# Performance work log

Hardware: AMD Instinct MI355X
Metric: run time of the kernel (lower is better)

Reference implementation:

```python
import jax, jax.numpy as jnp
import numpy as np

IN_FEATURES = 4096
OUT_FEATURES = 4096
BATCH, SEQ = 8, 2048


def setup_inputs() -> dict:
    key = jax.random.key(0)
    k1, k2, k3, k4 = jax.random.split(key, 4)
    x = jax.random.normal(k1, (BATCH, SEQ, IN_FEATURES), dtype=jnp.float32)
    # packed int4 weights: each int8 byte holds two signed 4-bit values
    weight = jax.random.randint(k2, (OUT_FEATURES, IN_FEATURES // 2), -128, 128, dtype=jnp.int8)
    # per-output-row symmetric quant scales (positive, small)
    scales = jax.random.uniform(k3, (OUT_FEATURES,), dtype=jnp.float32, minval=0.005, maxval=0.02)
    bias = jax.random.normal(k4, (OUT_FEATURES,), dtype=jnp.float32)
    return {"x": x, "weight": weight, "scales": scales, "bias": bias}


def _dequant_int4(weight, scales):
    # low nibble -> even input columns, high nibble -> odd input columns.
    # Arithmetic shifts on int8 sign-extend the 4-bit values.
    low = jnp.right_shift(jnp.left_shift(weight, 4), 4)   # (O, I/2) in [-8, 7]
    high = jnp.right_shift(weight, 4)                      # (O, I/2) in [-8, 7]
    w = jnp.stack([low, high], axis=-1).reshape(weight.shape[0], -1)  # (O, I)
    return w.astype(jnp.float32) * scales[:, None]


def reference(x, weight, scales, bias):
    W = _dequant_int4(weight, scales)                      # (O, I) fp32
    # y[b,s,o] = sum_i x[b,s,i] * W[o,i] + bias[o]
    return jnp.einsum('bsi,oi->bso', x, W) + bias
```

## Files before the change

kernel.cpp:

```cpp
#include <hip/hip_runtime.h>
#include <hip/hip_bf16.h>
#include <stdint.h>

#define M_TOTAL 16384
#define N_TOTAL 4096
#define K_TOTAL 4096

#define BM 256
#define BN 256
#define BKI 128
#define NTI (K_TOTAL / BKI)

typedef __attribute__((ext_vector_type(4))) float f32x4;
typedef __attribute__((ext_vector_type(4))) int   i32x4;
typedef __attribute__((ext_vector_type(2))) int   i32x2;

__global__ __launch_bounds__(256) void quant_x_kernel(
    const float* __restrict__ x, signed char* __restrict__ xq,
    float* __restrict__ qrow) {
  __shared__ float red[8];
  const int row = blockIdx.x;
  const int tid = threadIdx.x;
  const float* xr = x + (size_t)row * K_TOTAL;
  const f32x4* xv = (const f32x4*)xr;

  f32x4 v[4];
  float mx = 0.f;
#pragma unroll
  for (int j = 0; j < 4; ++j) {
    v[j] = xv[j * 256 + tid];
#pragma unroll
    for (int e = 0; e < 4; ++e) mx = fmaxf(mx, fabsf(v[j][e]));
  }
#pragma unroll
  for (int off = 32; off > 0; off >>= 1) mx = fmaxf(mx, __shfl_xor(mx, off));
  if ((tid & 63) == 0) red[tid >> 6] = mx;
  __syncthreads();
  if (tid == 0) {
    float m2 = fmaxf(fmaxf(red[0], red[1]), fmaxf(red[2], red[3]));
    red[4] = m2;
    qrow[row] = m2 * (1.f / 127.f);
  }
  __syncthreads();
  const float rmax = red[4];
  const float rq = rmax > 0.f ? 127.f / rmax : 0.f;

  int* oq = (int*)(xq + (size_t)row * K_TOTAL);
#pragma unroll
  for (int j = 0; j < 4; ++j) {
    int b0 = (int)rintf(v[j][0] * rq) & 0xff;
    int b1 = (int)rintf(v[j][1] * rq) & 0xff;
    int b2 = (int)rintf(v[j][2] * rq) & 0xff;
    int b3 = (int)rintf(v[j][3] * rq) & 0xff;
    oq[j * 256 + tid] = b0 | (b1 << 8) | (b2 << 16) | (b3 << 24);
  }
}

__global__ void dequant_w8_kernel(const int* __restrict__ wq,
                                  signed char* __restrict__ w8) {
  const int n = (N_TOTAL * (K_TOTAL / 2)) / 4;
  int idx = blockIdx.x * blockDim.x + threadIdx.x;
  int stride = gridDim.x * blockDim.x;
  const i32x4* wv = (const i32x4*)wq;
  i32x2* ov = (i32x2*)w8;
  for (int i = idx; i < n; i += stride) {
    i32x4 w = wv[i];
    int words[2];
#pragma unroll
    for (int h = 0; h < 2; ++h) {
      int b0 = w[2 * h], b1 = w[2 * h + 1];
      int lo0 = (((b0 & 0xF) ^ 8) - 8) & 0xff;
      int hi0 = ((((b0 >> 4) & 0xF) ^ 8) - 8) & 0xff;
      int lo1 = (((b1 & 0xF) ^ 8) - 8) & 0xff;
      int hi1 = ((((b1 >> 4) & 0xF) ^ 8) - 8) & 0xff;
      words[h] = lo0 | (hi0 << 8) | (lo1 << 16) | (hi1 << 24);
    }
    i32x2 o; o[0] = words[0]; o[1] = words[1];
    ov[i] = o;
  }
}

#define MFMAI(a, b, c) __builtin_amdgcn_mfma_i32_16x16x64_i8((a), (b), (c), 0, 0, 0)
#define SCHED0() __builtin_amdgcn_sched_barrier(0)

__global__ __launch_bounds__(512, 2) void gemm256_i8_kernel(
    const signed char* __restrict__ A8,
    const signed char* __restrict__ B8,
    const float* __restrict__ qrow,
    const float* __restrict__ scales,
    const float* __restrict__ bias,
    float* __restrict__ C) {
  __shared__ signed char lds[2][2][BM * BKI];

  const int t  = threadIdx.x;
  const int l  = t & 63;
  const int w  = t >> 6;
  const int wm = w >> 2;
  const int wn = w & 3;
  const int fr = l & 15;
  const int kg = l >> 4;
  const int sx = fr & 7;

  const int wg = blockIdx.x;
  const int bm = (wg & 7) * 8 + ((wg >> 3) & 7);
  const int bn = wg >> 6;

  const int rr   = t >> 3;
  const int ssrc = (t & 7) ^ (rr & 7);
  const signed char* pa = A8 + (size_t)(bm * BM + rr) * K_TOTAL + ssrc * 16;
  const signed char* pb = B8 + (size_t)(bn * BN + rr) * K_TOTAL + ssrc * 16;

#define GLL(gp, lp) __builtin_amdgcn_global_load_lds( \
      (const __attribute__((address_space(1))) unsigned int*)(gp), \
      (__attribute__((address_space(3))) unsigned int*)(lp), 16, 0, 0)

  auto stage = [&](int buf, int kt) {
#pragma unroll
    for (int g = 0; g < 4; ++g)
      GLL(pa + (size_t)g * 64 * K_TOTAL + kt, &lds[buf][0][g * 8192 + t * 16]);
#pragma unroll
    for (int g = 0; g < 4; ++g)
      GLL(pb + (size_t)g * 64 * K_TOTAL + kt, &lds[buf][1][g * 8192 + t * 16]);
  };

  i32x4 acc[8][4] = {};

  stage(0, 0);
  stage(1, BKI);

  const int so0 = (kg ^ sx) * 16;
  const int so1 = ((4 + kg) ^ sx) * 16;

  for (int t0 = 0; t0 < NTI; ++t0) {
    if (t0 == NTI - 1) { asm volatile("s_waitcnt vmcnt(0)" ::: "memory"); }
    else               { asm volatile("s_waitcnt vmcnt(8)" ::: "memory"); }
    SCHED0();
    __builtin_amdgcn_s_barrier();
    SCHED0();

    const int cur = t0 & 1;
    const signed char* Abp = &lds[cur][0][(wm * 128 + fr) * BKI];
    const signed char* Bbp = &lds[cur][1][(wn * 64 + fr) * BKI];

    i32x4 b[4][2], alo[4][2], ahi[4][2];
#pragma unroll
    for (int kk = 0; kk < 2; ++kk) {
      const int so = kk ? so1 : so0;
#pragma unroll
      for (int n = 0; n < 4; ++n) b[n][kk]   = *(const i32x4*)&Bbp[n * 16 * BKI + so];
#pragma unroll
      for (int m = 0; m < 4; ++m) alo[m][kk] = *(const i32x4*)&Abp[m * 16 * BKI + so];
    }
    SCHED0();
#pragma unroll
    for (int kk = 0; kk < 2; ++kk) {
      const int so = kk ? so1 : so0;
#pragma unroll
      for (int m = 0; m < 4; ++m) ahi[m][kk] = *(const i32x4*)&Abp[(m + 4) * 16 * BKI + so];
    }
    SCHED0();
    asm volatile("s_waitcnt lgkmcnt(8)" ::: "memory");
    SCHED0();
    __builtin_amdgcn_s_setprio(1);
#pragma unroll
    for (int kk = 0; kk < 2; ++kk)
#pragma unroll
      for (int m = 0; m < 4; ++m)
#pragma unroll
        for (int n = 0; n < 4; ++n)
          acc[m][n] = MFMAI(alo[m][kk], b[n][kk], acc[m][n]);
    __builtin_amdgcn_s_setprio(0);
    SCHED0();
    asm volatile("s_waitcnt lgkmcnt(0)" ::: "memory");
    SCHED0();
    __builtin_amdgcn_s_barrier();
    SCHED0();

    if (t0 + 2 < NTI) stage(cur, (t0 + 2) * BKI);

    __builtin_amdgcn_s_setprio(1);
#pragma unroll
    for (int kk = 0; kk < 2; ++kk)
#pragma unroll
      for (int m = 0; m < 4; ++m)
#pragma unroll
        for (int n = 0; n < 4; ++n)
          acc[m + 4][n] = MFMAI(ahi[m][kk], b[n][kk], acc[m + 4][n]);
    __builtin_amdgcn_s_setprio(0);
    SCHED0();
  }

  const int row0 = bm * BM + wm * 128 + kg * 4;
  const int col0 = bn * BN + wn * 64 + fr;
  float qv[8][4];
#pragma unroll
  for (int m = 0; m < 8; ++m)
#pragma unroll
    for (int r = 0; r < 4; ++r) qv[m][r] = qrow[row0 + m * 16 + r];
#pragma unroll
  for (int n = 0; n < 4; ++n) {
    const int gc = col0 + n * 16;
    const float s  = scales[gc];
    const float bv = bias[gc];
#pragma unroll
    for (int m = 0; m < 8; ++m) {
      const int gr = row0 + m * 16;
#pragma unroll
      for (int r = 0; r < 4; ++r)
        C[(size_t)(gr + r) * N_TOTAL + gc] = (float)acc[m][n][r] * (qv[m][r] * s) + bv;
    }
  }
#undef GLL
}

__global__ void naive_int4_kernel(const float* __restrict__ x,
                                  const int* __restrict__ wq,
                                  const float* __restrict__ scales,
                                  const float* __restrict__ bias,
                                  float* __restrict__ out) {
  size_t idx = (size_t)blockIdx.x * blockDim.x + threadIdx.x;
  int o = (int)(idx & (N_TOTAL - 1));
  int m = (int)(idx >> 12);
  const float* xr = x + (size_t)m * K_TOTAL;
  const int* wrow = wq + (size_t)o * (K_TOTAL / 2);
  float acc = 0.f;
  for (int j = 0; j < K_TOTAL / 2; ++j) {
    int b = wrow[j];
    int lo = ((b & 0xF) ^ 8) - 8;
    int hi = (((b >> 4) & 0xF) ^ 8) - 8;
    acc += xr[2 * j] * (float)lo + xr[2 * j + 1] * (float)hi;
  }
  out[idx] = acc * scales[o] + bias[o];
}

extern "C" void kernel_launch(void* const* d_in, const int* in_sizes, int n_in,
                              void* d_out, int out_size, void* d_ws, size_t ws_size,
                              hipStream_t stream) {
  const float* x      = (const float*)d_in[0];
  const int*   wq     = (const int*)d_in[1];
  const float* scales = (const float*)d_in[2];
  const float* bias   = (const float*)d_in[3];
  float* out = (float*)d_out;

  const size_t needXQ = (size_t)M_TOTAL * K_TOTAL;
  const size_t needW8 = (size_t)N_TOTAL * K_TOTAL;
  const size_t needQ  = (size_t)M_TOTAL * sizeof(float);

  if (d_ws != nullptr && ws_size >= needXQ + needW8 + needQ) {
    signed char* xq = (signed char*)d_ws;
    signed char* w8 = (signed char*)d_ws + needXQ;
    float* qrow = (float*)((char*)d_ws + needXQ + needW8);
    quant_x_kernel<<<M_TOTAL, 256, 0, stream>>>(x, xq, qrow);
    dequant_w8_kernel<<<1024, 256, 0, stream>>>(wq, w8);
    gemm256_i8_kernel<<<(M_TOTAL / BM) * (N_TOTAL / BN), 512, 0, stream>>>(
        xq, w8, qrow, scales, bias, out);
  } else {
    const size_t total = (size_t)M_TOTAL * N_TOTAL;
    naive_int4_kernel<<<(unsigned)(total / 256), 256, 0, stream>>>(x, wq, scales, bias, out);
  }
}
```

Baseline: 341.9 us.

## Load A operand directly from global into registers, stage only B in LDS

```diff
diff --git a/kernel.cpp b/kernel.cpp
--- a/kernel.cpp
+++ b/kernel.cpp
@@ -90,7 +90,7 @@
     const float* __restrict__ scales,
     const float* __restrict__ bias,
     float* __restrict__ C) {
-  __shared__ signed char lds[2][2][BM * BKI];
+  __shared__ signed char ldsB[2][BN * BKI];
 
   const int t  = threadIdx.x;
   const int l  = t & 63;
@@ -107,86 +107,101 @@
 
   const int rr   = t >> 3;
   const int ssrc = (t & 7) ^ (rr & 7);
-  const signed char* pa = A8 + (size_t)(bm * BM + rr) * K_TOTAL + ssrc * 16;
   const signed char* pb = B8 + (size_t)(bn * BN + rr) * K_TOTAL + ssrc * 16;
 
 #define GLL(gp, lp) __builtin_amdgcn_global_load_lds( \
       (const __attribute__((address_space(1))) unsigned int*)(gp), \
       (__attribute__((address_space(3))) unsigned int*)(lp), 16, 0, 0)
 
-  auto stage = [&](int buf, int kt) {
+  auto stageB = [&](int buf, int kt) {
 #pragma unroll
     for (int g = 0; g < 4; ++g)
-      GLL(pa + (size_t)g * 64 * K_TOTAL + kt, &lds[buf][0][g * 8192 + t * 16]);
-#pragma unroll
-    for (int g = 0; g < 4; ++g)
-      GLL(pb + (size_t)g * 64 * K_TOTAL + kt, &lds[buf][1][g * 8192 + t * 16]);
+      GLL(pb + (size_t)g * 64 * K_TOTAL + kt, &ldsB[buf][g * 8192 + t * 16]);
   };
 
+  const signed char* pA = A8 + (size_t)(bm * BM + wm * 128 + fr) * K_TOTAL + kg * 16;
+
   i32x4 acc[8][4] = {};
-
-  stage(0, 0);
-  stage(1, BKI);
+  i32x4 a0[8], a1[8], b[4][2];
+
+  stageB(0, 0);
+  stageB(1, BKI);
+#pragma unroll
+  for (int mf = 0; mf < 8; ++mf)
+    a0[mf] = *(const i32x4*)(pA + (size_t)mf * 16 * K_TOTAL);
+#pragma unroll
+  for (int mf = 0; mf < 8; ++mf)
+    a1[mf] = *(const i32x4*)(pA + (size_t)mf * 16 * K_TOTAL + 64);
+  SCHED0();
 
   const int so0 = (kg ^ sx) * 16;
   const int so1 = ((4 + kg) ^ sx) * 16;
 
   for (int t0 = 0; t0 < NTI; ++t0) {
-    if (t0 == NTI - 1) { asm volatile("s_waitcnt vmcnt(0)" ::: "memory"); }
-    else               { asm volatile("s_waitcnt vmcnt(8)" ::: "memory"); }
+    const bool hasNext = (t0 + 1 < NTI);
+    const size_t ktn = (size_t)(t0 + 1) * BKI;
+
+    asm volatile("s_waitcnt vmcnt(16)" ::: "memory");
     SCHED0();
     __builtin_amdgcn_s_barrier();
     SCHED0();
 
     const int cur = t0 & 1;
-    const signed char* Abp = &lds[cur][0][(wm * 128 + fr) * BKI];
-    const signed char* Bbp = &lds[cur][1][(wn * 64 + fr) * BKI];
-
-    i32x4 b[4][2], alo[4][2], ahi[4][2];
-#pragma unroll
-    for (int kk = 0; kk < 2; ++kk) {
-      const int so = kk ? so1 : so0;
-#pragma unroll
-      for (int n = 0; n < 4; ++n) b[n][kk]   = *(const i32x4*)&Bbp[n * 16 * BKI + so];
-#pragma unroll
-      for (int m = 0; m < 4; ++m) alo[m][kk] = *(const i32x4*)&Abp[m * 16 * BKI + so];
-    }
-    SCHED0();
-#pragma unroll
-    for (int kk = 0; kk < 2; ++kk) {
-      const int so = kk ? so1 : so0;
-#pragma unroll
-      for (int m = 0; m < 4; ++m) ahi[m][kk] = *(const i32x4*)&Abp[(m + 4) * 16 * BKI + so];
-    }
-    SCHED0();
-    asm volatile("s_waitcnt lgkmcnt(8)" ::: "memory");
-    SCHED0();
+    const signed char* Bbp = &ldsB[cur][(wn * 64 + fr) * BKI];
+
+#pragma unroll
+    for (int n = 0; n < 4; ++n) b[n][0] = *(const i32x4*)&Bbp[n * 16 * BKI + so0];
+    SCHED0();
+#pragma unroll
+    for (int n = 0; n < 4; ++n) b[n][1] = *(const i32x4*)&Bbp[n * 16 * BKI + so1];
+    SCHED0();
+
     __builtin_amdgcn_s_setprio(1);
 #pragma unroll
-    for (int kk = 0; kk < 2; ++kk)
-#pragma unroll
-      for (int m = 0; m < 4; ++m)
-#pragma unroll
-        for (int n = 0; n < 4; ++n)
-          acc[m][n] = MFMAI(alo[m][kk], b[n][kk], acc[m][n]);
+    for (int m = 0; m < 8; ++m)
+#pragma unroll
+      for (int n = 0; n < 4; ++n)
+        acc[m][n] = MFMAI(a0[m], b[n][0], acc[m][n]);
     __builtin_amdgcn_s_setprio(0);
     SCHED0();
+
+    if (hasNext) {
+#pragma unroll
+      for (int mf = 0; mf < 8; ++mf)
+        a0[mf] = *(const i32x4*)(pA + (size_t)mf * 16 * K_TOTAL + ktn);
+    }
+    SCHED0();
+
+    __builtin_amdgcn_s_setprio(1);
+#pragma unroll
+    for (int m = 0; m < 8; ++m)
+#pragma unroll
+      for (int n = 0; n < 4; ++n)
+        acc[m][n + 0] = acc[m][n];
+    __builtin_amdgcn_s_setprio(0);
+#pragma unroll
+    for (int m = 0; m < 8; ++m) { }
+    __builtin_amdgcn_s_setprio(1);
+#pragma unroll
+    for (int m = 0; m < 8; ++m)
+#pragma unroll
+      for (int n = 0; n < 4; ++n)
+        acc[m][n] = MFMAI(a1[m], b[n][1], acc[m][n]);
+    __builtin_amdgcn_s_setprio(0);
+    SCHED0();
+
     asm volatile("s_waitcnt lgkmcnt(0)" ::: "memory");
     SCHED0();
     __builtin_amdgcn_s_barrier();
     SCHED0();
 
-    if (t0 + 2 < NTI) stage(cur, (t0 + 2) * BKI);
-
-    __builtin_amdgcn_s_setprio(1);
-#pragma unroll
-    for (int kk = 0; kk < 2; ++kk)
-#pragma unroll
-      for (int m = 0; m < 4; ++m)
-#pragma unroll
-        for (int n = 0; n < 4; ++n)
-          acc[m + 4][n] = MFMAI(ahi[m][kk], b[n][kk], acc[m + 4][n]);
-    __builtin_amdgcn_s_setprio(0);
+    if (t0 + 2 < NTI) stageB(cur, (size_t)(t0 + 2) * BKI);
+    SCHED0();
+    if (hasNext) {
+#pragma unroll
+      for (int mf = 0; mf < 8; ++mf)
+        a1[mf] = *(const i32x4*)(pA + (size_t)mf * 16 * K_TOTAL + ktn + 64);
+    }
     SCHED0();
   }
 
```

After: 636.7 us. 86.2% more time.

## Switch int8 GEMM to 4-stage pipeline with 64-wide K tiles and one barrier

Applied to the files above, without the earlier changes.

```diff
diff --git a/kernel.cpp b/kernel.cpp
--- a/kernel.cpp
+++ b/kernel.cpp
@@ -8,7 +8,7 @@
 
 #define BM 256
 #define BN 256
-#define BKI 128
+#define BKI 64
 #define NTI (K_TOTAL / BKI)
 
 typedef __attribute__((ext_vector_type(4))) float f32x4;
@@ -90,7 +90,7 @@
     const float* __restrict__ scales,
     const float* __restrict__ bias,
     float* __restrict__ C) {
-  __shared__ signed char lds[2][2][BM * BKI];
+  __shared__ signed char lds[4][2][BM * BKI];
 
   const int t  = threadIdx.x;
   const int l  = t & 63;
@@ -99,96 +99,71 @@
   const int wn = w & 3;
   const int fr = l & 15;
   const int kg = l >> 4;
-  const int sx = fr & 7;
+  const int sxs = (kg ^ ((fr >> 1) & 3)) << 4;
 
   const int wg = blockIdx.x;
   const int bm = (wg & 7) * 8 + ((wg >> 3) & 7);
   const int bn = wg >> 6;
 
-  const int rr   = t >> 3;
-  const int ssrc = (t & 7) ^ (rr & 7);
-  const signed char* pa = A8 + (size_t)(bm * BM + rr) * K_TOTAL + ssrc * 16;
-  const signed char* pb = B8 + (size_t)(bn * BN + rr) * K_TOTAL + ssrc * 16;
+  const int rr   = t >> 2;
+  const int ssrc = ((t & 3) ^ ((t >> 3) & 3)) << 4;
+  const signed char* pa = A8 + (size_t)(bm * BM + rr) * K_TOTAL + ssrc;
+  const signed char* pb = B8 + (size_t)(bn * BN + rr) * K_TOTAL + ssrc;
 
 #define GLL(gp, lp) __builtin_amdgcn_global_load_lds( \
       (const __attribute__((address_space(1))) unsigned int*)(gp), \
       (__attribute__((address_space(3))) unsigned int*)(lp), 16, 0, 0)
 
-  auto stage = [&](int buf, int kt) {
-#pragma unroll
-    for (int g = 0; g < 4; ++g)
-      GLL(pa + (size_t)g * 64 * K_TOTAL + kt, &lds[buf][0][g * 8192 + t * 16]);
-#pragma unroll
-    for (int g = 0; g < 4; ++g)
-      GLL(pb + (size_t)g * 64 * K_TOTAL + kt, &lds[buf][1][g * 8192 + t * 16]);
+  auto stage = [&](int slot, size_t kt) {
+    GLL(pa + kt,                           &lds[slot][0][t * 16]);
+    GLL(pa + (size_t)128 * K_TOTAL + kt,   &lds[slot][0][8192 + t * 16]);
+    GLL(pb + kt,                           &lds[slot][1][t * 16]);
+    GLL(pb + (size_t)128 * K_TOTAL + kt,   &lds[slot][1][8192 + t * 16]);
   };
 
   i32x4 acc[8][4] = {};
 
-  stage(0, 0);
-  stage(1, BKI);
-
-  const int so0 = (kg ^ sx) * 16;
-  const int so1 = ((4 + kg) ^ sx) * 16;
-
-  for (int t0 = 0; t0 < NTI; ++t0) {
-    if (t0 == NTI - 1) { asm volatile("s_waitcnt vmcnt(0)" ::: "memory"); }
-    else               { asm volatile("s_waitcnt vmcnt(8)" ::: "memory"); }
-    SCHED0();
-    __builtin_amdgcn_s_barrier();
-    SCHED0();
-
-    const int cur = t0 & 1;
-    const signed char* Abp = &lds[cur][0][(wm * 128 + fr) * BKI];
-    const signed char* Bbp = &lds[cur][1][(wn * 64 + fr) * BKI];
-
-    i32x4 b[4][2], alo[4][2], ahi[4][2];
-#pragma unroll
-    for (int kk = 0; kk < 2; ++kk) {
-      const int so = kk ? so1 : so0;
-#pragma unroll
-      for (int n = 0; n < 4; ++n) b[n][kk]   = *(const i32x4*)&Bbp[n * 16 * BKI + so];
-#pragma unroll
-      for (int m = 0; m < 4; ++m) alo[m][kk] = *(const i32x4*)&Abp[m * 16 * BKI + so];
-    }
-    SCHED0();
-#pragma unroll
-    for (int kk = 0; kk < 2; ++kk) {
-      const int so = kk ? so1 : so0;
-#pragma unroll
-      for (int m = 0; m < 4; ++m) ahi[m][kk] = *(const i32x4*)&Abp[(m + 4) * 16 * BKI + so];
-    }
-    SCHED0();
-    asm volatile("s_waitcnt lgkmcnt(8)" ::: "memory");
-    SCHED0();
-    __builtin_amdgcn_s_setprio(1);
-#pragma unroll
-    for (int kk = 0; kk < 2; ++kk)
-#pragma unroll
-      for (int m = 0; m < 4; ++m)
-#pragma unroll
-        for (int n = 0; n < 4; ++n)
-          acc[m][n] = MFMAI(alo[m][kk], b[n][kk], acc[m][n]);
-    __builtin_amdgcn_s_setprio(0);
-    SCHED0();
-    asm volatile("s_waitcnt lgkmcnt(0)" ::: "memory");
-    SCHED0();
-    __builtin_amdgcn_s_barrier();
-    SCHED0();
-
-    if (t0 + 2 < NTI) stage(cur, (t0 + 2) * BKI);
-
-    __builtin_amdgcn_s_setprio(1);
-#pragma unroll
-    for (int kk = 0; kk < 2; ++kk)
-#pragma unroll
-      for (int m = 0; m < 4; ++m)
-#pragma unroll
-        for (int n = 0; n < 4; ++n)
-          acc[m + 4][n] = MFMAI(ahi[m][kk], b[n][kk], acc[m + 4][n]);
-    __builtin_amdgcn_s_setprio(0);
-    SCHED0();
-  }
+  const int abase = (wm * 128 + fr) * BKI + sxs;
+  const int bbase = (wn * 64 + fr) * BKI + sxs;
+
+  stage(0, 0); stage(1, BKI); stage(2, 2 * BKI);
+  asm volatile("s_waitcnt vmcnt(8)" ::: "memory");
+  SCHED0();
+  __builtin_amdgcn_s_barrier();
+  SCHED0();
+
+#define TILE_BODY(T0, DOSTAGE, VMASM) do {                                   \
+    const signed char* Ab = &lds[(T0) & 3][0][abase];                        \
+    const signed char* Bb = &lds[(T0) & 3][1][bbase];                        \
+    i32x4 a_[8], b_[4];                                                      \
+    _Pragma("unroll")                                                        \
+    for (int mf = 0; mf < 8; ++mf) a_[mf] = *(const i32x4*)&Ab[mf * 16 * BKI]; \
+    _Pragma("unroll")                                                        \
+    for (int nf = 0; nf < 4; ++nf) b_[nf] = *(const i32x4*)&Bb[nf * 16 * BKI]; \
+    SCHED0();                                                                \
+    if (DOSTAGE) stage(((T0) + 3) & 3, (size_t)((T0) + 3) * BKI);            \
+    SCHED0();                                                                \
+    asm volatile(VMASM ::: "memory");                                        \
+    asm volatile("s_waitcnt lgkmcnt(0)" ::: "memory");                       \
+    SCHED0();                                                                \
+    __builtin_amdgcn_s_barrier();                                            \
+    SCHED0();                                                                \
+    __builtin_amdgcn_s_setprio(1);                                           \
+    _Pragma("unroll")                                                        \
+    for (int mf = 0; mf < 8; ++mf)                                           \
+      _Pragma("unroll")                                                      \
+      for (int nf = 0; nf < 4; ++nf)                                         \
+        acc[mf][nf] = MFMAI(a_[mf], b_[nf], acc[mf][nf]);                    \
+    __builtin_amdgcn_s_setprio(0);                                           \
+    SCHED0();                                                                \
+  } while (0)
+
+  for (int t0 = 0; t0 < NTI - 3; ++t0)
+    TILE_BODY(t0, true, "s_waitcnt vmcnt(8)");
+  TILE_BODY(NTI - 3, false, "s_waitcnt vmcnt(4)");
+  TILE_BODY(NTI - 2, false, "s_waitcnt vmcnt(0)");
+  TILE_BODY(NTI - 1, false, "s_waitcnt vmcnt(0)");
+#undef TILE_BODY
 
   const int row0 = bm * BM + wm * 128 + kg * 4;
   const int col0 = bn * BN + wn * 64 + fr;
```

Result: slower. 353.0 us (+3.2%).

## Pre-pack B into MFMA fragment order and load it directly from global

Applied to the files above, without the earlier changes.

```diff
diff --git a/kernel.cpp b/kernel.cpp
--- a/kernel.cpp
+++ b/kernel.cpp
@@ -8,12 +8,11 @@
 
 #define BM 256
 #define BN 256
-#define BKI 128
+#define BKI 64
 #define NTI (K_TOTAL / BKI)
 
 typedef __attribute__((ext_vector_type(4))) float f32x4;
 typedef __attribute__((ext_vector_type(4))) int   i32x4;
-typedef __attribute__((ext_vector_type(2))) int   i32x2;
 
 __global__ __launch_bounds__(256) void quant_x_kernel(
     const float* __restrict__ x, signed char* __restrict__ xq,
@@ -56,27 +55,37 @@
   }
 }
 
-__global__ void dequant_w8_kernel(const int* __restrict__ wq,
-                                  signed char* __restrict__ w8) {
-  const int n = (N_TOTAL * (K_TOTAL / 2)) / 4;
-  int idx = blockIdx.x * blockDim.x + threadIdx.x;
-  int stride = gridDim.x * blockDim.x;
-  const i32x4* wv = (const i32x4*)wq;
-  i32x2* ov = (i32x2*)w8;
-  for (int i = idx; i < n; i += stride) {
-    i32x4 w = wv[i];
-    int words[2];
+__global__ __launch_bounds__(256) void dequant_pack_kernel(
+    const int* __restrict__ wq, signed char* __restrict__ Bp) {
+  const int u0 = (blockIdx.x * 256 + threadIdx.x) * 4;
+#pragma unroll
+  for (int i = 0; i < 4; ++i) {
+    const int u = u0 + i;
+    const int lane = u & 63;
+    const int nf = (u >> 6) & 7;
+    const int tt = (u >> 9) & 63;
+    const int wnb = u >> 15;
+    const int o = (wnb >> 1) * 256 + (wnb & 1) * 128 + nf * 16 + (lane & 15);
+    const int k = tt * 64 + (lane >> 4) * 16;
+    const int* src = wq + (size_t)o * (K_TOTAL / 2) + (k >> 1);
+    i32x4 s0 = *(const i32x4*)src;
+    i32x4 s1 = *(const i32x4*)(src + 4);
+    int wds[4];
 #pragma unroll
     for (int h = 0; h < 2; ++h) {
-      int b0 = w[2 * h], b1 = w[2 * h + 1];
-      int lo0 = (((b0 & 0xF) ^ 8) - 8) & 0xff;
-      int hi0 = ((((b0 >> 4) & 0xF) ^ 8) - 8) & 0xff;
-      int lo1 = (((b1 & 0xF) ^ 8) - 8) & 0xff;
-      int hi1 = ((((b1 >> 4) & 0xF) ^ 8) - 8) & 0xff;
-      words[h] = lo0 | (hi0 << 8) | (lo1 << 16) | (hi1 << 24);
+      i32x4 s = h ? s1 : s0;
+#pragma unroll
+      for (int p = 0; p < 2; ++p) {
+        int ba = s[2 * p], bb = s[2 * p + 1];
+        int lo0 = (((ba & 0xF) ^ 8) - 8) & 0xff;
+        int hi0 = ((((ba >> 4) & 0xF) ^ 8) - 8) & 0xff;
+        int lo1 = (((bb & 0xF) ^ 8) - 8) & 0xff;
+        int hi1 = ((((bb >> 4) & 0xF) ^ 8) - 8) & 0xff;
+        wds[h * 2 + p] = lo0 | (hi0 << 8) | (lo1 << 16) | (hi1 << 24);
+      }
     }
-    i32x2 o; o[0] = words[0]; o[1] = words[1];
-    ov[i] = o;
+    i32x4 o4; o4[0] = wds[0]; o4[1] = wds[1]; o4[2] = wds[2]; o4[3] = wds[3];
+    *(i32x4*)(Bp + (size_t)u * 16) = o4;
   }
 }
 
@@ -85,129 +94,98 @@
 
 __global__ __launch_bounds__(512, 2) void gemm256_i8_kernel(
     const signed char* __restrict__ A8,
-    const signed char* __restrict__ B8,
+    const signed char* __restrict__ Bp,
     const float* __restrict__ qrow,
     const float* __restrict__ scales,
     const float* __restrict__ bias,
     float* __restrict__ C) {
-  __shared__ signed char lds[2][2][BM * BKI];
+  __shared__ signed char ldsA[4][BM * BKI];
 
   const int t  = threadIdx.x;
   const int l  = t & 63;
   const int w  = t >> 6;
-  const int wm = w >> 2;
-  const int wn = w & 3;
+  const int wm = w >> 1;
+  const int wn = w & 1;
   const int fr = l & 15;
   const int kg = l >> 4;
-  const int sx = fr & 7;
+  const int sxs = (kg ^ ((fr >> 1) & 3)) << 4;
 
   const int wg = blockIdx.x;
   const int bm = (wg & 7) * 8 + ((wg >> 3) & 7);
   const int bn = wg >> 6;
 
-  const int rr   = t >> 3;
-  const int ssrc = (t & 7) ^ (rr & 7);
-  const signed char* pa = A8 + (size_t)(bm * BM + rr) * K_TOTAL + ssrc * 16;
-  const signed char* pb = B8 + (size_t)(bn * BN + rr) * K_TOTAL + ssrc * 16;
+  const int rr   = t >> 2;
+  const int ssrc = ((t & 3) ^ ((t >> 3) & 3)) << 4;
+  const signed char* pa = A8 + (size_t)(bm * BM + rr) * K_TOTAL + ssrc;
 
 #define GLL(gp, lp) __builtin_amdgcn_global_load_lds( \
       (const __attribute__((address_space(1))) unsigned int*)(gp), \
       (__attribute__((address_space(3))) unsigned int*)(lp), 16, 0, 0)
 
-  auto stage = [&](int buf, int kt) {
-#pragma unroll
-    for (int g = 0; g < 4; ++g)
-      GLL(pa + (size_t)g * 64 * K_TOTAL + kt, &lds[buf][0][g * 8192 + t * 16]);
-#pragma unroll
-    for (int g = 0; g < 4; ++g)
-      GLL(pb + (size_t)g * 64 * K_TOTAL + kt, &lds[buf][1][g * 8192 + t * 16]);
+  auto stageA = [&](int slot, size_t kt) {
+    GLL(pa + kt,                         &ldsA[slot][t * 16]);
+    GLL(pa + (size_t)128 * K_TOTAL + kt, &ldsA[slot][8192 + t * 16]);
   };
 
-  i32x4 acc[8][4] = {};
-
-  stage(0, 0);
-  stage(1, BKI);
-
-  const int so0 = (kg ^ sx) * 16;
-  const int so1 = ((4 + kg) ^ sx) * 16;
+  const signed char* pB = Bp + (size_t)(bn * 2 + wn) * 524288 + l * 16;
+
+  i32x4 acc[4][8] = {};
+  i32x4 a_[4], b_[8];
+
+  stageA(0, 0); stageA(1, BKI);
+  asm volatile("s_waitcnt vmcnt(2)" ::: "memory");
+  SCHED0();
+
+  const int abase = (wm * 64 + fr) * BKI + sxs;
 
   for (int t0 = 0; t0 < NTI; ++t0) {
-    if (t0 == NTI - 1) { asm volatile("s_waitcnt vmcnt(0)" ::: "memory"); }
-    else               { asm volatile("s_waitcnt vmcnt(8)" ::: "memory"); }
     SCHED0();
     __builtin_amdgcn_s_barrier();
     SCHED0();
-
-    const int cur = t0 & 1;
-    const signed char* Abp = &lds[cur][0][(wm * 128 + fr) * BKI];
-    const signed char* Bbp = &lds[cur][1][(wn * 64 + fr) * BKI];
-
-    i32x4 b[4][2], alo[4][2], ahi[4][2];
-#pragma unroll
-    for (int kk = 0; kk < 2; ++kk) {
-      const int so = kk ? so1 : so0;
-#pragma unroll
-      for (int n = 0; n < 4; ++n) b[n][kk]   = *(const i32x4*)&Bbp[n * 16 * BKI + so];
-#pragma unroll
-      for (int m = 0; m < 4; ++m) alo[m][kk] = *(const i32x4*)&Abp[m * 16 * BKI + so];
-    }
-    SCHED0();
-#pragma unroll
-    for (int kk = 0; kk < 2; ++kk) {
-      const int so = kk ? so1 : so0;
-#pragma unroll
-      for (int m = 0; m < 4; ++m) ahi[m][kk] = *(const i32x4*)&Abp[(m + 4) * 16 * BKI + so];
-    }
-    SCHED0();
-    asm volatile("s_waitcnt lgkmcnt(8)" ::: "memory");
+    const signed char* pBt = pB + (size_t)t0 * 8192;
+#pragma unroll
+    for (int nf = 0; nf < 8; ++nf)
+      b_[nf] = *(const i32x4*)(pBt + nf * 1024);
+    SCHED0();
+    const signed char* Ab = &ldsA[t0 & 3][abase];
+#pragma unroll
+    for (int mf = 0; mf < 4; ++mf)
+      a_[mf] = *(const i32x4*)&Ab[mf * 16 * BKI];
+    SCHED0();
+    if (t0 + 2 < NTI) stageA((t0 + 2) & 3, (size_t)(t0 + 2) * BKI);
+    SCHED0();
+    asm volatile("s_waitcnt lgkmcnt(0)" ::: "memory");
+    if (t0 < NTI - 2) { asm volatile("s_waitcnt vmcnt(2)" ::: "memory"); }
+    else              { asm volatile("s_waitcnt vmcnt(0)" ::: "memory"); }
     SCHED0();
     __builtin_amdgcn_s_setprio(1);
 #pragma unroll
-    for (int kk = 0; kk < 2; ++kk)
-#pragma unroll
-      for (int m = 0; m < 4; ++m)
-#pragma unroll
-        for (int n = 0; n < 4; ++n)
-          acc[m][n] = MFMAI(alo[m][kk], b[n][kk], acc[m][n]);
+    for (int mf = 0; mf < 4; ++mf)
+#pragma unroll
+      for (int nf = 0; nf < 8; ++nf)
+        acc[mf][nf] = MFMAI(a_[mf], b_[nf], acc[mf][nf]);
     __builtin_amdgcn_s_setprio(0);
     SCHED0();
-    asm volatile("s_waitcnt lgkmcnt(0)" ::: "memory");
-    SCHED0();
-    __builtin_amdgcn_s_barrier();
-    SCHED0();
-
-    if (t0 + 2 < NTI) stage(cur, (t0 + 2) * BKI);
-
-    __builtin_amdgcn_s_setprio(1);
-#pragma unroll
-    for (int kk = 0; kk < 2; ++kk)
-#pragma unroll
-      for (int m = 0; m < 4; ++m)
-#pragma unroll
-        for (int n = 0; n < 4; ++n)
-          acc[m + 4][n] = MFMAI(ahi[m][kk], b[n][kk], acc[m + 4][n]);
-    __builtin_amdgcn_s_setprio(0);
-    SCHED0();
-  }
-
-  const int row0 = bm * BM + wm * 128 + kg * 4;
-  const int col0 = bn * BN + wn * 64 + fr;
-  float qv[8][4];
-#pragma unroll
-  for (int m = 0; m < 8; ++m)
+  }
+
+  const int row0 = bm * BM + wm * 64 + kg * 4;
+  const int col0 = bn * BN + wn * 128 + fr;
+  float qv[4][4];
+#pragma unroll
+  for (int m = 0; m < 4; ++m)
 #pragma unroll
     for (int r = 0; r < 4; ++r) qv[m][r] = qrow[row0 + m * 16 + r];
 #pragma unroll
-  for (int n = 0; n < 4; ++n) {
-    const int gc = col0 + n * 16;
+  for (int nf = 0; nf < 8; ++nf) {
+    const int gc = col0 + nf * 16;
     const float s  = scales[gc];
     const float bv = bias[gc];
 #pragma unroll
-    for (int m = 0; m < 8; ++m) {
+    for (int m = 0; m < 4; ++m) {
       const int gr = row0 + m * 16;
 #pragma unroll
       for (int r = 0; r < 4; ++r)
-        C[(size_t)(gr + r) * N_TOTAL + gc] = (float)acc[m][n][r] * (qv[m][r] * s) + bv;
+        C[(size_t)(gr + r) * N_TOTAL + gc] = (float)acc[m][nf][r] * (qv[m][r] * s) + bv;
     }
   }
 #undef GLL
@@ -248,12 +226,12 @@
 
   if (d_ws != nullptr && ws_size >= needXQ + needW8 + needQ) {
     signed char* xq = (signed char*)d_ws;
-    signed char* w8 = (signed char*)d_ws + needXQ;
+    signed char* bp = (signed char*)d_ws + needXQ;
     float* qrow = (float*)((char*)d_ws + needXQ + needW8);
     quant_x_kernel<<<M_TOTAL, 256, 0, stream>>>(x, xq, qrow);
-    dequant_w8_kernel<<<1024, 256, 0, stream>>>(wq, w8);
+    dequant_pack_kernel<<<1024, 256, 0, stream>>>(wq, bp);
     gemm256_i8_kernel<<<(M_TOTAL / BM) * (N_TOTAL / BN), 512, 0, stream>>>(
-        xq, w8, qrow, scales, bias, out);
+        xq, bp, qrow, scales, bias, out);
   } else {
     const size_t total = (size_t)M_TOTAL * N_TOTAL;
     naive_int4_kernel<<<(unsigned)(total / 256), 256, 0, stream>>>(x, wq, scales, bias, out);
```

New measurement: 456.2 us. +33.4%, slower.
